# Kernel optimization log

Measured on AMD Instinct MI355X. Metric: run time of the kernel, lower is better.

Reference implementation:

```python
import jax, jax.numpy as jnp
import numpy as np

DT = 0.01
MIN_VARIANCE = 0.01
REG_WEIGHT = 0.01
EPS = 1e-06


def setup_inputs() -> dict:
    key = jax.random.key(0)
    k1, k2, k3, k4 = jax.random.split(key, 4)
    B, T = 256, 16384
    return {
        "vel_pred": jax.random.normal(k1, (B, T, 2), dtype=jnp.float32),
        "cov_pred": jax.random.normal(k2, (B, T, 2), dtype=jnp.float32),
        "vel_gt": jax.random.normal(k3, (B, T, 2), dtype=jnp.float32),
        "pos_gt": jax.random.normal(k4, (B, T, 2), dtype=jnp.float32),
        "log_delta_v": jnp.zeros((), dtype=jnp.float32),
        "log_delta_c": jnp.zeros((), dtype=jnp.float32),
    }


def reference(vel_pred, cov_pred, vel_gt, pos_gt, log_delta_v, log_delta_c):
    # Sequential loop pos[t] = pos[t-1] + vel_pred[t-1]*dt, pos[0] = vel_pred[0]*dt
    # == dt * (vel_pred[:, 0:1] + exclusive_cumsum_T(vel_pred))  -- a parallel scan.
    excl = jnp.concatenate(
        [jnp.zeros_like(vel_pred[:, :1]), jnp.cumsum(vel_pred[:, :-1], axis=1)], axis=1
    )
    pos_pred = (vel_pred[:, :1] + excl) * DT  # [B, T, 2]

    lv_p = jnp.mean((pos_pred - pos_gt) ** 2)
    lv_e = jnp.mean((vel_pred - vel_gt) ** 2)
    lv_total = lv_p + lv_e

    sigma = jnp.clip(jnp.exp(cov_pred), MIN_VARIANCE, None)  # [B, T, 2] diag cov
    inv_sigma = 1.0 / sigma
    diff = vel_gt - vel_pred
    mahal = jnp.sum(inv_sigma * diff ** 2, axis=-1)  # [B, T]
    log_det = jnp.log(sigma[..., 0] * sigma[..., 1] + EPS)
    lc_total = 0.5 * jnp.mean(mahal + log_det)

    delta_v = jnp.exp(log_delta_v)
    delta_c = jnp.exp(log_delta_c)
    total_loss = (
        lv_total / (2.0 * delta_v ** 2)
        + lc_total / (2.0 * delta_c ** 2)
        + log_delta_v
        + log_delta_c
    )
    reg = jnp.mean(jnp.sum(inv_sigma, axis=-1))
    total_loss = total_loss + REG_WEIGHT * reg
    return total_loss
```

## Files before the change

kernel.cpp:

```cpp
#include <hip/hip_runtime.h>

static constexpr int B_ = 256;
static constexpr int T_ = 16384;
static constexpr int THREADS = 256;
static constexpr int SEG_T = 2048;
static constexpr int NSEG = T_ / SEG_T;
static constexpr int NBLK = B_ * NSEG;
static constexpr int F4_PER_ROW = T_ * 2 / 4;
static constexpr int F4_PER_SEG = SEG_T * 2 / 4;
static constexpr int F4_PER_THR = F4_PER_SEG / THREADS;

static constexpr float DTc    = 0.01f;
static constexpr float MINVAR = 0.01f;
static constexpr float EPSc   = 1e-6f;


__device__ __forceinline__ float waveReduce(float v) {
#pragma unroll
  for (int d = 32; d > 0; d >>= 1) v += __shfl_down(v, d, 64);
  return v;
}

__device__ __forceinline__ double waveReduceD(double v) {
#pragma unroll
  for (int d = 32; d > 0; d >>= 1) v += __shfl_down(v, d, 64);
  return v;
}

__global__ __launch_bounds__(THREADS) void kernA(
    const float4* __restrict__ vel, const float4* __restrict__ cov,
    const float4* __restrict__ vgt, float2* __restrict__ segsum,
    float* __restrict__ pLve, float* __restrict__ pLc, float* __restrict__ pReg) {
  const int bid = blockIdx.x;
  const int b = bid >> 3, s = bid & (NSEG - 1);
  const int tid = threadIdx.x;
  const int base = b * F4_PER_ROW + s * F4_PER_SEG + tid * F4_PER_THR;

  float4 v[4], c[4], g[4];
#pragma unroll
  for (int i = 0; i < 4; ++i) v[i] = vel[base + i];
#pragma unroll
  for (int i = 0; i < 4; ++i) c[i] = cov[base + i];
#pragma unroll
  for (int i = 0; i < 4; ++i) g[i] = vgt[base + i];

  float sumx = 0.f, sumy = 0.f;
  float lve = 0.f, lc = 0.f, reg = 0.f;
#pragma unroll
  for (int i = 0; i < 4; ++i) {
    sumx += v[i].x + v[i].z;
    sumy += v[i].y + v[i].w;
    {
      float dx = g[i].x - v[i].x, dy = g[i].y - v[i].y;
      float sqx = dx * dx, sqy = dy * dy;
      lve += sqx + sqy;
      float sx = fmaxf(__expf(c[i].x), MINVAR);
      float sy = fmaxf(__expf(c[i].y), MINVAR);
      float ix = 1.0f / sx, iy = 1.0f / sy;
      lc += ix * sqx + iy * sqy + __logf(sx * sy + EPSc);
      reg += ix + iy;
    }
    {
      float dx = g[i].z - v[i].z, dy = g[i].w - v[i].w;
      float sqx = dx * dx, sqy = dy * dy;
      lve += sqx + sqy;
      float sx = fmaxf(__expf(c[i].z), MINVAR);
      float sy = fmaxf(__expf(c[i].w), MINVAR);
      float ix = 1.0f / sx, iy = 1.0f / sy;
      lc += ix * sqx + iy * sqy + __logf(sx * sy + EPSc);
      reg += ix + iy;
    }
  }

  const int lane = tid & 63, wid = tid >> 6;
  float rx = waveReduce(sumx);
  float ry = waveReduce(sumy);
  float r1 = waveReduce(lve);
  float r2 = waveReduce(lc);
  float r3 = waveReduce(reg);
  __shared__ float sh[5][4];
  if (lane == 0) { sh[0][wid] = rx; sh[1][wid] = ry; sh[2][wid] = r1; sh[3][wid] = r2; sh[4][wid] = r3; }
  __syncthreads();
  if (tid == 0) {
    segsum[bid] = make_float2(sh[0][0] + sh[0][1] + sh[0][2] + sh[0][3],
                              sh[1][0] + sh[1][1] + sh[1][2] + sh[1][3]);
    pLve[bid] = sh[2][0] + sh[2][1] + sh[2][2] + sh[2][3];
    pLc [bid] = sh[3][0] + sh[3][1] + sh[3][2] + sh[3][3];
    pReg[bid] = sh[4][0] + sh[4][1] + sh[4][2] + sh[4][3];
  }
}

__global__ __launch_bounds__(THREADS) void kernB(
    const float4* __restrict__ vel, const float4* __restrict__ pgt,
    const float2* __restrict__ segsum, float* __restrict__ pPos) {
  const int bid = blockIdx.x;
  const int b = bid >> 3, s = bid & (NSEG - 1);
  const int tid = threadIdx.x;
  const int lane = tid & 63, wid = tid >> 6;
  const int base = b * F4_PER_ROW + s * F4_PER_SEG + tid * F4_PER_THR;

  float4 v[4], g[4];
#pragma unroll
  for (int i = 0; i < 4; ++i) v[i] = vel[base + i];
#pragma unroll
  for (int i = 0; i < 4; ++i) g[i] = pgt[base + i];

  float csx = 0.f, csy = 0.f;
#pragma unroll
  for (int i = 0; i < 4; ++i) { csx += v[i].x + v[i].z; csy += v[i].y + v[i].w; }

  float ix = csx, iy = csy;
#pragma unroll
  for (int d = 1; d < 64; d <<= 1) {
    float tx = __shfl_up(ix, (unsigned)d, 64);
    float ty = __shfl_up(iy, (unsigned)d, 64);
    if (lane >= d) { ix += tx; iy += ty; }
  }
  __shared__ float2 wtot[4];
  if (lane == 63) wtot[wid] = make_float2(ix, iy);
  __syncthreads();

  float bx = ix - csx, by = iy - csy;
  for (int w = 0; w < wid; ++w) { bx += wtot[w].x; by += wtot[w].y; }

  const float2* ss = segsum + b * NSEG;
  for (int k = 0; k < s; ++k) { float2 t = ss[k]; bx += t.x; by += t.y; }

  const float2 v0 = ((const float2*)vel)[b * T_];

  float apos = 0.f;
#pragma unroll
  for (int i = 0; i < 4; ++i) {
    float px = DTc * (v0.x + bx), py = DTc * (v0.y + by);
    float ex = px - g[i].x, ey = py - g[i].y;
    apos += ex * ex + ey * ey;
    bx += v[i].x; by += v[i].y;
    px = DTc * (v0.x + bx); py = DTc * (v0.y + by);
    ex = px - g[i].z; ey = py - g[i].w;
    apos += ex * ex + ey * ey;
    bx += v[i].z; by += v[i].w;
  }

  float r = waveReduce(apos);
  __shared__ float sh[4];
  if (lane == 0) sh[wid] = r;
  __syncthreads();
  if (tid == 0) pPos[bid] = sh[0] + sh[1] + sh[2] + sh[3];
}

__global__ __launch_bounds__(THREADS) void kernC(
    const float* __restrict__ pLve, const float* __restrict__ pLc,
    const float* __restrict__ pReg, const float* __restrict__ pPos,
    const float* __restrict__ pldv, const float* __restrict__ pldc,
    float* __restrict__ out) {
  const int tid = threadIdx.x;
  const int lane = tid & 63, wid = tid >> 6;
  double a0 = 0.0, a1 = 0.0, a2 = 0.0, a3 = 0.0;
#pragma unroll
  for (int i = 0; i < NBLK / THREADS; ++i) {
    int idx = tid + i * THREADS;
    a0 += (double)pPos[idx];
    a1 += (double)pLve[idx];
    a2 += (double)pLc[idx];
    a3 += (double)pReg[idx];
  }
  a0 = waveReduceD(a0);
  a1 = waveReduceD(a1);
  a2 = waveReduceD(a2);
  a3 = waveReduceD(a3);
  __shared__ double sh[4][4];
  if (lane == 0) { sh[0][wid] = a0; sh[1][wid] = a1; sh[2][wid] = a2; sh[3][wid] = a3; }
  __syncthreads();
  if (tid == 0) {
    double pos_sq = sh[0][0] + sh[0][1] + sh[0][2] + sh[0][3];
    double vel_sq = sh[1][0] + sh[1][1] + sh[1][2] + sh[1][3];
    double lcs    = sh[2][0] + sh[2][1] + sh[2][2] + sh[2][3];
    double regs   = sh[3][0] + sh[3][1] + sh[3][2] + sh[3][3];
    const double NBT2 = (double)B_ * (double)T_ * 2.0;
    const double NBT  = (double)B_ * (double)T_;
    double lv  = (pos_sq + vel_sq) / NBT2;
    double lc  = 0.5 * lcs / NBT;
    double reg = regs / NBT;
    double ldv = (double)pldv[0], ldc = (double)pldc[0];
    double total = lv / (2.0 * exp(2.0 * ldv)) + lc / (2.0 * exp(2.0 * ldc))
                 + ldv + ldc + 0.01 * reg;
    out[0] = (float)total;
  }
}

extern "C" void kernel_launch(void* const* d_in, const int* in_sizes, int n_in,
                              void* d_out, int out_size, void* d_ws, size_t ws_size,
                              hipStream_t stream) {
  const float4* vel = (const float4*)d_in[0];
  const float4* cov = (const float4*)d_in[1];
  const float4* vgt = (const float4*)d_in[2];
  const float4* pgt = (const float4*)d_in[3];
  const float* ldv = (const float*)d_in[4];
  const float* ldc = (const float*)d_in[5];

  char* ws = (char*)d_ws;
  float2* segsum = (float2*)ws;
  float* pLve = (float*)(ws + 16 * 1024);
  float* pLc  = (float*)(ws + 24 * 1024);
  float* pReg = (float*)(ws + 32 * 1024);
  float* pPos = (float*)(ws + 40 * 1024);

  kernA<<<NBLK, THREADS, 0, stream>>>(vel, cov, vgt, segsum, pLve, pLc, pReg);
  kernB<<<NBLK, THREADS, 0, stream>>>(vel, pgt, segsum, pPos);
  kernC<<<1, THREADS, 0, stream>>>(pLve, pLc, pReg, pPos, ldv, ldc, (float*)d_out);
}
```

Baseline: 159.3 us.

## Coalesce global loads with strided per-thread access and an LDS-based segment scan

Each thread now loads float4s strided by the block size instead of four contiguous float4s, so a wavefront's accesses are fully coalesced on every load instruction. In kernB, the scan order is recovered by writing per-float4 pair sums to shared memory, scanning contiguous groups of four per thread plus a wave/block scan, then writing exclusive prefixes back to LDS for the strided consumers. This adds two extra barriers and LDS traffic in exchange for better memory access patterns in a bandwidth-bound kernel.

```diff
diff --git a/kernel.cpp b/kernel.cpp
--- a/kernel.cpp
+++ b/kernel.cpp
@@ -8,7 +8,6 @@
 static constexpr int NBLK = B_ * NSEG;
 static constexpr int F4_PER_ROW = T_ * 2 / 4;
 static constexpr int F4_PER_SEG = SEG_T * 2 / 4;
-static constexpr int F4_PER_THR = F4_PER_SEG / THREADS;
 
 static constexpr float DTc    = 0.01f;
 static constexpr float MINVAR = 0.01f;
@@ -34,15 +33,15 @@
   const int bid = blockIdx.x;
   const int b = bid >> 3, s = bid & (NSEG - 1);
   const int tid = threadIdx.x;
-  const int base = b * F4_PER_ROW + s * F4_PER_SEG + tid * F4_PER_THR;
+  const int base = b * F4_PER_ROW + s * F4_PER_SEG + tid;
 
   float4 v[4], c[4], g[4];
 #pragma unroll
-  for (int i = 0; i < 4; ++i) v[i] = vel[base + i];
-#pragma unroll
-  for (int i = 0; i < 4; ++i) c[i] = cov[base + i];
-#pragma unroll
-  for (int i = 0; i < 4; ++i) g[i] = vgt[base + i];
+  for (int i = 0; i < 4; ++i) v[i] = vel[base + i * THREADS];
+#pragma unroll
+  for (int i = 0; i < 4; ++i) c[i] = cov[base + i * THREADS];
+#pragma unroll
+  for (int i = 0; i < 4; ++i) g[i] = vgt[base + i * THREADS];
 
   float sumx = 0.f, sumy = 0.f;
   float lve = 0.f, lc = 0.f, reg = 0.f;
@@ -97,40 +96,56 @@
   const int b = bid >> 3, s = bid & (NSEG - 1);
   const int tid = threadIdx.x;
   const int lane = tid & 63, wid = tid >> 6;
-  const int base = b * F4_PER_ROW + s * F4_PER_SEG + tid * F4_PER_THR;
+  const int base = b * F4_PER_ROW + s * F4_PER_SEG + tid;
 
   float4 v[4], g[4];
 #pragma unroll
-  for (int i = 0; i < 4; ++i) v[i] = vel[base + i];
-#pragma unroll
-  for (int i = 0; i < 4; ++i) g[i] = pgt[base + i];
-
-  float csx = 0.f, csy = 0.f;
-#pragma unroll
-  for (int i = 0; i < 4; ++i) { csx += v[i].x + v[i].z; csy += v[i].y + v[i].w; }
-
-  float ix = csx, iy = csy;
+  for (int i = 0; i < 4; ++i) v[i] = vel[base + i * THREADS];
+#pragma unroll
+  for (int i = 0; i < 4; ++i) g[i] = pgt[base + i * THREADS];
+
+  __shared__ float2 ps[F4_PER_SEG];
+#pragma unroll
+  for (int i = 0; i < 4; ++i)
+    ps[tid + i * THREADS] = make_float2(v[i].x + v[i].z, v[i].y + v[i].w);
+  __syncthreads();
+
+  float2 e0 = ps[4 * tid + 0], e1 = ps[4 * tid + 1], e2 = ps[4 * tid + 2], e3 = ps[4 * tid + 3];
+  float i1x = e0.x + e1.x,   i1y = e0.y + e1.y;
+  float i2x = i1x + e2.x,    i2y = i1y + e2.y;
+  float tx  = i2x + e3.x,    ty  = i2y + e3.y;
+
+  float sxv = tx, syv = ty;
 #pragma unroll
   for (int d = 1; d < 64; d <<= 1) {
-    float tx = __shfl_up(ix, (unsigned)d, 64);
-    float ty = __shfl_up(iy, (unsigned)d, 64);
-    if (lane >= d) { ix += tx; iy += ty; }
-  }
-  __shared__ float2 wtot[4];
-  if (lane == 63) wtot[wid] = make_float2(ix, iy);
-  __syncthreads();
-
-  float bx = ix - csx, by = iy - csy;
-  for (int w = 0; w < wid; ++w) { bx += wtot[w].x; by += wtot[w].y; }
-
+    float ux = __shfl_up(sxv, (unsigned)d, 64);
+    float uy = __shfl_up(syv, (unsigned)d, 64);
+    if (lane >= d) { sxv += ux; syv += uy; }
+  }
+  __shared__ float2 wt[4];
+  if (lane == 63) wt[wid] = make_float2(sxv, syv);
+  __syncthreads();
+
+  float offx = sxv - tx, offy = syv - ty;
+  for (int w = 0; w < wid; ++w) { offx += wt[w].x; offy += wt[w].y; }
+
+  ps[4 * tid + 0] = make_float2(offx,        offy);
+  ps[4 * tid + 1] = make_float2(offx + e0.x, offy + e0.y);
+  ps[4 * tid + 2] = make_float2(offx + i1x,  offy + i1y);
+  ps[4 * tid + 3] = make_float2(offx + i2x,  offy + i2y);
+  __syncthreads();
+
+  float rxo = 0.f, ryo = 0.f;
   const float2* ss = segsum + b * NSEG;
-  for (int k = 0; k < s; ++k) { float2 t = ss[k]; bx += t.x; by += t.y; }
+  for (int k = 0; k < s; ++k) { float2 t2 = ss[k]; rxo += t2.x; ryo += t2.y; }
 
   const float2 v0 = ((const float2*)vel)[b * T_];
 
   float apos = 0.f;
 #pragma unroll
   for (int i = 0; i < 4; ++i) {
+    float2 p = ps[tid + i * THREADS];
+    float bx = p.x + rxo, by = p.y + ryo;
     float px = DTc * (v0.x + bx), py = DTc * (v0.y + by);
     float ex = px - g[i].x, ey = py - g[i].y;
     apos += ex * ex + ey * ey;
@@ -138,7 +153,6 @@
     px = DTc * (v0.x + bx); py = DTc * (v0.y + by);
     ex = px - g[i].z; ey = py - g[i].w;
     apos += ex * ex + ey * ey;
-    bx += v[i].z; by += v[i].w;
   }
 
   float r = waveReduce(apos);
```

Result: no change. 158.3 us (-0.7%).

## Fuse stats and scan kernels into one row-per-block chunked scan

Applied to the files above, without the earlier changes.

Replaces the two-pass segment-sum plus scan kernels with a single kernel where each 1024-thread block walks a full row in chunks, carrying a running prefix and prefetching the next chunk into registers. This removes the second read of the velocity array and one kernel launch, and it simplifies the final reduction to one value per row. In exchange, the grid shrinks to one block per row, and there is a barrier per chunk, which may reduce memory-level parallelism.

```diff
diff --git a/kernel.cpp b/kernel.cpp
--- a/kernel.cpp
+++ b/kernel.cpp
@@ -2,13 +2,9 @@
 
 static constexpr int B_ = 256;
 static constexpr int T_ = 16384;
-static constexpr int THREADS = 256;
-static constexpr int SEG_T = 2048;
-static constexpr int NSEG = T_ / SEG_T;
-static constexpr int NBLK = B_ * NSEG;
-static constexpr int F4_PER_ROW = T_ * 2 / 4;
-static constexpr int F4_PER_SEG = SEG_T * 2 / 4;
-static constexpr int F4_PER_THR = F4_PER_SEG / THREADS;
+static constexpr int TPB = 1024;
+static constexpr int F4_ROW = T_ * 2 / 4;
+static constexpr int CHUNKS = F4_ROW / TPB;
 
 static constexpr float DTc    = 0.01f;
 static constexpr float MINVAR = 0.01f;
@@ -20,150 +16,125 @@
   for (int d = 32; d > 0; d >>= 1) v += __shfl_down(v, d, 64);
   return v;
 }
-
 __device__ __forceinline__ double waveReduceD(double v) {
 #pragma unroll
   for (int d = 32; d > 0; d >>= 1) v += __shfl_down(v, d, 64);
   return v;
 }
 
-__global__ __launch_bounds__(THREADS) void kernA(
+__global__ __launch_bounds__(TPB) void fusedKern(
     const float4* __restrict__ vel, const float4* __restrict__ cov,
-    const float4* __restrict__ vgt, float2* __restrict__ segsum,
-    float* __restrict__ pLve, float* __restrict__ pLc, float* __restrict__ pReg) {
-  const int bid = blockIdx.x;
-  const int b = bid >> 3, s = bid & (NSEG - 1);
+    const float4* __restrict__ vgt, const float4* __restrict__ pgt,
+    float* __restrict__ pPos, float* __restrict__ pLve,
+    float* __restrict__ pLc,  float* __restrict__ pReg) {
+  const int b = blockIdx.x;
   const int tid = threadIdx.x;
-  const int base = b * F4_PER_ROW + s * F4_PER_SEG + tid * F4_PER_THR;
+  const int lane = tid & 63, wid = tid >> 6;
+  const int rowbase = b * F4_ROW;
 
-  float4 v[4], c[4], g[4];
-#pragma unroll
-  for (int i = 0; i < 4; ++i) v[i] = vel[base + i];
-#pragma unroll
-  for (int i = 0; i < 4; ++i) c[i] = cov[base + i];
-#pragma unroll
-  for (int i = 0; i < 4; ++i) g[i] = vgt[base + i];
+  __shared__ float2 wt[2][16];
+  __shared__ float  sh[4][16];
 
-  float sumx = 0.f, sumy = 0.f;
-  float lve = 0.f, lc = 0.f, reg = 0.f;
-#pragma unroll
-  for (int i = 0; i < 4; ++i) {
-    sumx += v[i].x + v[i].z;
-    sumy += v[i].y + v[i].w;
+  const float2 v0 = ((const float2*)vel)[b * T_];
+
+  float runx = 0.f, runy = 0.f;
+  float lve = 0.f, lc = 0.f, reg = 0.f, apos = 0.f;
+
+  float4 v = vel[rowbase + tid];
+  float4 c = cov[rowbase + tid];
+  float4 g = vgt[rowbase + tid];
+  float4 p = pgt[rowbase + tid];
+
+  for (int ch = 0; ch < CHUNKS; ++ch) {
+    float4 nv, nc, ng, np;
+    const bool more = (ch + 1 < CHUNKS);
+    if (more) {
+      int idx = rowbase + (ch + 1) * TPB + tid;
+      nv = vel[idx]; nc = cov[idx]; ng = vgt[idx]; np = pgt[idx];
+    }
+
     {
-      float dx = g[i].x - v[i].x, dy = g[i].y - v[i].y;
+      float dx = g.x - v.x, dy = g.y - v.y;
       float sqx = dx * dx, sqy = dy * dy;
       lve += sqx + sqy;
-      float sx = fmaxf(__expf(c[i].x), MINVAR);
-      float sy = fmaxf(__expf(c[i].y), MINVAR);
-      float ix = 1.0f / sx, iy = 1.0f / sy;
-      lc += ix * sqx + iy * sqy + __logf(sx * sy + EPSc);
-      reg += ix + iy;
+      float sx = fmaxf(__expf(c.x), MINVAR);
+      float sy = fmaxf(__expf(c.y), MINVAR);
+      float ixv = 1.0f / sx, iyv = 1.0f / sy;
+      lc += ixv * sqx + iyv * sqy + __logf(sx * sy + EPSc);
+      reg += ixv + iyv;
     }
     {
-      float dx = g[i].z - v[i].z, dy = g[i].w - v[i].w;
+      float dx = g.z - v.z, dy = g.w - v.w;
       float sqx = dx * dx, sqy = dy * dy;
       lve += sqx + sqy;
-      float sx = fmaxf(__expf(c[i].z), MINVAR);
-      float sy = fmaxf(__expf(c[i].w), MINVAR);
-      float ix = 1.0f / sx, iy = 1.0f / sy;
-      lc += ix * sqx + iy * sqy + __logf(sx * sy + EPSc);
-      reg += ix + iy;
+      float sx = fmaxf(__expf(c.z), MINVAR);
+      float sy = fmaxf(__expf(c.w), MINVAR);
+      float ixv = 1.0f / sx, iyv = 1.0f / sy;
+      lc += ixv * sqx + iyv * sqy + __logf(sx * sy + EPSc);
+      reg += ixv + iyv;
     }
+
+    const float sx = v.x + v.z, sy = v.y + v.w;
+    float ix = sx, iy = sy;
+#pragma unroll
+    for (int d = 1; d < 64; d <<= 1) {
+      float ux = __shfl_up(ix, (unsigned)d, 64);
+      float uy = __shfl_up(iy, (unsigned)d, 64);
+      if (lane >= d) { ix += ux; iy += uy; }
+    }
+    const int slot = ch & 1;
+    if (lane == 63) wt[slot][wid] = make_float2(ix, iy);
+    __syncthreads();
+
+    float offx = ix - sx + runx, offy = iy - sy + runy;
+    float ctx = 0.f, cty = 0.f;
+#pragma unroll
+    for (int w = 0; w < 16; ++w) {
+      float2 t = wt[slot][w];
+      if (w < wid) { offx += t.x; offy += t.y; }
+      ctx += t.x; cty += t.y;
+    }
+
+    {
+      float px = DTc * (v0.x + offx), py = DTc * (v0.y + offy);
+      float ex = px - p.x, ey = py - p.y;
+      apos += ex * ex + ey * ey;
+      float bx2 = offx + v.x, by2 = offy + v.y;
+      px = DTc * (v0.x + bx2); py = DTc * (v0.y + by2);
+      ex = px - p.z; ey = py - p.w;
+      apos += ex * ex + ey * ey;
+    }
+
+    runx += ctx; runy += cty;
+    if (more) { v = nv; c = nc; g = ng; p = np; }
   }
 
-  const int lane = tid & 63, wid = tid >> 6;
-  float rx = waveReduce(sumx);
-  float ry = waveReduce(sumy);
+  float r0 = waveReduce(apos);
   float r1 = waveReduce(lve);
   float r2 = waveReduce(lc);
   float r3 = waveReduce(reg);
-  __shared__ float sh[5][4];
-  if (lane == 0) { sh[0][wid] = rx; sh[1][wid] = ry; sh[2][wid] = r1; sh[3][wid] = r2; sh[4][wid] = r3; }
+  __syncthreads();
+  if (lane == 0) { sh[0][wid] = r0; sh[1][wid] = r1; sh[2][wid] = r2; sh[3][wid] = r3; }
   __syncthreads();
   if (tid == 0) {
-    segsum[bid] = make_float2(sh[0][0] + sh[0][1] + sh[0][2] + sh[0][3],
-                              sh[1][0] + sh[1][1] + sh[1][2] + sh[1][3]);
-    pLve[bid] = sh[2][0] + sh[2][1] + sh[2][2] + sh[2][3];
-    pLc [bid] = sh[3][0] + sh[3][1] + sh[3][2] + sh[3][3];
-    pReg[bid] = sh[4][0] + sh[4][1] + sh[4][2] + sh[4][3];
+    float t0 = 0.f, t1 = 0.f, t2 = 0.f, t3 = 0.f;
+#pragma unroll
+    for (int w = 0; w < 16; ++w) { t0 += sh[0][w]; t1 += sh[1][w]; t2 += sh[2][w]; t3 += sh[3][w]; }
+    pPos[b] = t0; pLve[b] = t1; pLc[b] = t2; pReg[b] = t3;
   }
 }
 
-__global__ __launch_bounds__(THREADS) void kernB(
-    const float4* __restrict__ vel, const float4* __restrict__ pgt,
-    const float2* __restrict__ segsum, float* __restrict__ pPos) {
-  const int bid = blockIdx.x;
-  const int b = bid >> 3, s = bid & (NSEG - 1);
-  const int tid = threadIdx.x;
-  const int lane = tid & 63, wid = tid >> 6;
-  const int base = b * F4_PER_ROW + s * F4_PER_SEG + tid * F4_PER_THR;
-
-  float4 v[4], g[4];
-#pragma unroll
-  for (int i = 0; i < 4; ++i) v[i] = vel[base + i];
-#pragma unroll
-  for (int i = 0; i < 4; ++i) g[i] = pgt[base + i];
-
-  float csx = 0.f, csy = 0.f;
-#pragma unroll
-  for (int i = 0; i < 4; ++i) { csx += v[i].x + v[i].z; csy += v[i].y + v[i].w; }
-
-  float ix = csx, iy = csy;
-#pragma unroll
-  for (int d = 1; d < 64; d <<= 1) {
-    float tx = __shfl_up(ix, (unsigned)d, 64);
-    float ty = __shfl_up(iy, (unsigned)d, 64);
-    if (lane >= d) { ix += tx; iy += ty; }
-  }
-  __shared__ float2 wtot[4];
-  if (lane == 63) wtot[wid] = make_float2(ix, iy);
-  __syncthreads();
-
-  float bx = ix - csx, by = iy - csy;
-  for (int w = 0; w < wid; ++w) { bx += wtot[w].x; by += wtot[w].y; }
-
-  const float2* ss = segsum + b * NSEG;
-  for (int k = 0; k < s; ++k) { float2 t = ss[k]; bx += t.x; by += t.y; }
-
-  const float2 v0 = ((const float2*)vel)[b * T_];
-
-  float apos = 0.f;
-#pragma unroll
-  for (int i = 0; i < 4; ++i) {
-    float px = DTc * (v0.x + bx), py = DTc * (v0.y + by);
-    float ex = px - g[i].x, ey = py - g[i].y;
-    apos += ex * ex + ey * ey;
-    bx += v[i].x; by += v[i].y;
-    px = DTc * (v0.x + bx); py = DTc * (v0.y + by);
-    ex = px - g[i].z; ey = py - g[i].w;
-    apos += ex * ex + ey * ey;
-    bx += v[i].z; by += v[i].w;
-  }
-
-  float r = waveReduce(apos);
-  __shared__ float sh[4];
-  if (lane == 0) sh[wid] = r;
-  __syncthreads();
-  if (tid == 0) pPos[bid] = sh[0] + sh[1] + sh[2] + sh[3];
-}
-
-__global__ __launch_bounds__(THREADS) void kernC(
-    const float* __restrict__ pLve, const float* __restrict__ pLc,
-    const float* __restrict__ pReg, const float* __restrict__ pPos,
+__global__ __launch_bounds__(256) void kernC(
+    const float* __restrict__ pPos, const float* __restrict__ pLve,
+    const float* __restrict__ pLc,  const float* __restrict__ pReg,
     const float* __restrict__ pldv, const float* __restrict__ pldc,
     float* __restrict__ out) {
   const int tid = threadIdx.x;
   const int lane = tid & 63, wid = tid >> 6;
-  double a0 = 0.0, a1 = 0.0, a2 = 0.0, a3 = 0.0;
-#pragma unroll
-  for (int i = 0; i < NBLK / THREADS; ++i) {
-    int idx = tid + i * THREADS;
-    a0 += (double)pPos[idx];
-    a1 += (double)pLve[idx];
-    a2 += (double)pLc[idx];
-    a3 += (double)pReg[idx];
-  }
+  double a0 = (double)pPos[tid];
+  double a1 = (double)pLve[tid];
+  double a2 = (double)pLc[tid];
+  double a3 = (double)pReg[tid];
   a0 = waveReduceD(a0);
   a1 = waveReduceD(a1);
   a2 = waveReduceD(a2);
@@ -199,13 +170,11 @@
   const float* ldc = (const float*)d_in[5];
 
   char* ws = (char*)d_ws;
-  float2* segsum = (float2*)ws;
-  float* pLve = (float*)(ws + 16 * 1024);
-  float* pLc  = (float*)(ws + 24 * 1024);
-  float* pReg = (float*)(ws + 32 * 1024);
-  float* pPos = (float*)(ws + 40 * 1024);
+  float* pPos = (float*)ws;
+  float* pLve = (float*)(ws + 1024);
+  float* pLc  = (float*)(ws + 2048);
+  float* pReg = (float*)(ws + 3072);
 
-  kernA<<<NBLK, THREADS, 0, stream>>>(vel, cov, vgt, segsum, pLve, pLc, pReg);
-  kernB<<<NBLK, THREADS, 0, stream>>>(vel, pgt, segsum, pPos);
-  kernC<<<1, THREADS, 0, stream>>>(pLve, pLc, pReg, pPos, ldv, ldc, (float*)d_out);
+  fusedKern<<<B_, TPB, 0, stream>>>(vel, cov, vgt, pgt, pPos, pLve, pLc, pReg);
+  kernC<<<1, 256, 0, stream>>>(pPos, pLve, pLc, pReg, ldv, ldc, (float*)d_out);
 }
```

Result: no change. 159.8 us (+0.3%).
